# Optimization experiments

Hardware: AMD Instinct MI355X
Metric: run time of the kernel (lower is better)

## Reference

```python
import jax, jax.numpy as jnp
import numpy as np

N_HEADS = 16
N_KV_HEADS = 4
WINDOW = 128
THETA = 10000.0


def _rope_cos_sin(T, half):
    inv = 1.0 / (THETA ** (jnp.arange(half, dtype=jnp.float32) / half))
    f = jnp.arange(T, dtype=jnp.float32)[:, None] * inv[None, :]  # (T, half)
    return jnp.cos(f), jnp.sin(f)


def _apply_rope(x, cos, sin):
    # x: (B, H, T, hd); interleaved (real, imag) pairs like torch view_as_complex
    xr, xi = x[..., 0::2], x[..., 1::2]
    out_r = xr * cos - xi * sin
    out_i = xr * sin + xi * cos
    return jnp.stack([out_r, out_i], axis=-1).reshape(x.shape)


def setup_inputs() -> dict:
    key = jax.random.key(0)
    ks = jax.random.split(key, 6)
    B, T, C = 1, 4096, 2048
    kvC = (C // N_HEADS) * N_KV_HEADS
    return {
        "x": jax.random.normal(ks[0], (B, T, C), dtype=jnp.float32),
        "wq": jax.random.normal(ks[1], (C, C), dtype=jnp.float32) * 0.02,
        "wk": jax.random.normal(ks[2], (C, kvC), dtype=jnp.float32) * 0.02,
        "wv": jax.random.normal(ks[3], (C, kvC), dtype=jnp.float32) * 0.02,
        "wo": jax.random.normal(ks[4], (C, C), dtype=jnp.float32) * 0.02,
        "sink": jnp.zeros((1, N_HEADS, 1, 1), dtype=jnp.float32),
    }


def reference(x, wq, wk, wv, wo, sink):
    B, T, C = x.shape
    hd = C // N_HEADS
    n_rep = N_HEADS // N_KV_HEADS

    q = (x @ wq).reshape(B, T, N_HEADS, hd).transpose(0, 2, 1, 3)    # (B,H,T,hd)
    k = (x @ wk).reshape(B, T, N_KV_HEADS, hd).transpose(0, 2, 1, 3)  # (B,Hkv,T,hd)
    v = (x @ wv).reshape(B, T, N_KV_HEADS, hd).transpose(0, 2, 1, 3)

    cos, sin = _rope_cos_sin(T, hd // 2)  # (T, hd/2), broadcasts over (B,H,T,hd/2)
    q = _apply_rope(q, cos, sin)
    k = _apply_rope(k, cos, sin)

    # GQA head expansion (repeat_interleave over head dim)
    k = jnp.repeat(k, n_rep, axis=1)
    v = jnp.repeat(v, n_rep, axis=1)

    att = jnp.einsum("bhqd,bhkd->bhqk", q, k) * (hd ** -0.5) + sink

    # symmetric sliding-window band: |i - j| <= window//2
    idx = jnp.arange(T)
    band = jnp.abs(idx[:, None] - idx[None, :]) <= (WINDOW // 2)
    att = jnp.where(band[None, None, :, :], att, -jnp.inf)

    att = jax.nn.softmax(att, axis=-1)
    # torch code replaces NaN rows (fully-masked) with uniform; band always has diag so no-op
    att = jnp.where(jnp.isnan(att), 1.0 / T, att)

    out = jnp.einsum("bhqk,bhkd->bqhd", att, v).reshape(B, T, C)
    return out @ wo
```

## Files before the change

kernel.cpp:

```cpp
#include <hip/hip_runtime.h>
#include <stdint.h>

#define T_SEQ 4096
#define C_DIM 2048
#define HD 128

typedef unsigned short ushort_t;
typedef __attribute__((ext_vector_type(8))) short shortx8;
typedef __attribute__((ext_vector_type(4))) float floatx4;
typedef __attribute__((ext_vector_type(8))) unsigned short u16x8;
typedef __attribute__((ext_vector_type(4))) unsigned short u16x4;

__device__ __forceinline__ ushort_t f2bf(float f) {
  union { float f; uint32_t u; } v; v.f = f;
  v.u += 0x7fffu + ((v.u >> 16) & 1u);
  return (ushort_t)(v.u >> 16);
}
__device__ __forceinline__ void load_lds16(const ushort_t* g, ushort_t* l) {
  __builtin_amdgcn_global_load_lds(
      (const __attribute__((address_space(1))) unsigned int*)g,
      (__attribute__((address_space(3))) unsigned int*)l, 16, 0, 0);
}

__global__ __launch_bounds__(256) void prep_kernel(
    const float* __restrict__ wq, const float* __restrict__ wk,
    const float* __restrict__ wv, const float* __restrict__ wo,
    const float* __restrict__ x,
    ushort_t* __restrict__ BtAll, ushort_t* __restrict__ woT,
    ushort_t* __restrict__ xb) {
  const int bid = blockIdx.x;
  const int tid = threadIdx.x;
  if (bid >= 2560) {
    int i = (bid - 2560) * 256 + tid;
    float4 v = ((const float4*)x)[i];
    u16x4 o; o[0] = f2bf(v.x); o[1] = f2bf(v.y); o[2] = f2bf(v.z); o[3] = f2bf(v.w);
    ((u16x4*)xb)[i] = o;
    return;
  }
  const float* src; ushort_t* dst; int C, bx, by;
  if (bid < 1024) { src = wq; dst = BtAll; C = 2048; bx = bid & 31; by = bid >> 5; }
  else if (bid < 1280) { int b = bid - 1024; src = wk; dst = BtAll + (size_t)2048 * 2048; C = 512; bx = b & 7; by = b >> 3; }
  else if (bid < 1536) { int b = bid - 1280; src = wv; dst = BtAll + (size_t)2560 * 2048; C = 512; bx = b & 7; by = b >> 3; }
  else { int b = bid - 1536; src = wo; dst = woT; C = 2048; bx = b & 31; by = b >> 5; }
  const int R = 2048;

  __shared__ float tile[64][65];
  const int c0 = bx * 64, r0 = by * 64;
  for (int i = tid; i < 1024; i += 256) {
    int r = i >> 4, cc = (i & 15) * 4;
    float4 v = *(const float4*)&src[(size_t)(r0 + r) * C + c0 + cc];
    tile[r][cc] = v.x; tile[r][cc + 1] = v.y; tile[r][cc + 2] = v.z; tile[r][cc + 3] = v.w;
  }
  __syncthreads();
  for (int i = tid; i < 512; i += 256) {
    int oc = i >> 3;
    int g = (i & 7) * 8;
    u16x8 o;
    for (int j = 0; j < 8; ++j) o[j] = f2bf(tile[g + j][oc]);
    *(u16x8*)&dst[(size_t)(c0 + oc) * R + r0 + g] = o;
  }
}


struct GemmAcc { floatx4 a[4][4]; };

__device__ __forceinline__ void gemm_core_bk64(
    const ushort_t* __restrict__ A, const ushort_t* __restrict__ Bt,
    ushort_t* As, ushort_t* Bs, GemmAcc& acc,
    int m0, int n0, int K, int tid, int lane, int wave, int quad, int l16,
    int wm, int wn) {
  const int nk = K >> 6;
  for (int kk = 0; kk < nk; ++kk) {
    const int k0 = kk << 6;
    for (int r = 0; r < 4; ++r) {
      int e = r * 256 + tid;
      int row = e >> 3;
      int p = e & 7;
      int g = (p - row) & 7;
      const ushort_t* ga = A + (size_t)(m0 + row) * K + k0 + g * 8;
      const ushort_t* gb = Bt + (size_t)(n0 + row) * K + k0 + g * 8;
      ushort_t* la = As + (size_t)(r * 256 + (tid & 192)) * 8;
      ushort_t* lb = Bs + (size_t)(r * 256 + (tid & 192)) * 8;
      load_lds16(ga, la);
      load_lds16(gb, lb);
    }
    __syncthreads();
    for (int ks = 0; ks < 2; ++ks) {
      shortx8 af[4], bfr[4];
      for (int i = 0; i < 4; ++i) {
        int ar = wm + i * 16 + l16;
        af[i] = *(const shortx8*)(As + ar * 64 + (((ks << 2) + quad + ar) & 7) * 8);
        int br = wn + i * 16 + l16;
        bfr[i] = *(const shortx8*)(Bs + br * 64 + (((ks << 2) + quad + br) & 7) * 8);
      }
      for (int i = 0; i < 4; ++i)
        for (int j = 0; j < 4; ++j)
          acc.a[i][j] = __builtin_amdgcn_mfma_f32_16x16x32_bf16(af[i], bfr[j], acc.a[i][j], 0, 0, 0);
    }
    __syncthreads();
  }
}

__global__ __launch_bounds__(256, 3) void gemm_qkv(
    const ushort_t* __restrict__ A, const ushort_t* __restrict__ Bt,
    ushort_t* __restrict__ qbb, ushort_t* __restrict__ kbb,
    ushort_t* __restrict__ vtb) {
  __shared__ __align__(16) ushort_t As[128 * 64];
  __shared__ __align__(16) ushort_t Bs[128 * 64];
  const int tid = threadIdx.x;
  const int lane = tid & 63;
  const int wave = tid >> 6;
  const int quad = lane >> 4;
  const int l16 = lane & 15;
  const int m0 = blockIdx.y * 128;
  const int n0 = blockIdx.x * 128;
  const int wm = (wave & 1) * 64;
  const int wn = (wave >> 1) * 64;

  GemmAcc acc = {};
  gemm_core_bk64(A, Bt, As, Bs, acc, m0, n0, 2048, tid, lane, wave, quad, l16, wm, wn);

  if (blockIdx.x < 20) {
    const bool isq = (blockIdx.x < 16);
    const int par = l16 & 1;
    for (int j = 0; j < 4; ++j) {
      int col = n0 + wn + j * 16 + l16;
      int irot = (col & 127) >> 1;
      float inv = __expf(-0.14391157f * (float)irot);
      for (int i = 0; i < 4; ++i) {
        int t0r = m0 + wm + i * 16 + quad * 4;
        for (int r = 0; r < 4; ++r) {
          float val = acc.a[i][j][r];
          float other = __shfl_xor(val, 1, 64);
          float sn, cs;
          __sincosf((float)(t0r + r) * inv, &sn, &cs);
          float outv = par ? (other * sn + val * cs) : (val * cs - other * sn);
          if (isq) qbb[(size_t)(t0r + r) * 2048 + col] = f2bf(outv);
          else     kbb[(size_t)(t0r + r) * 512 + (col - 2048)] = f2bf(outv);
        }
      }
    }
  } else {
    for (int j = 0; j < 4; ++j) {
      int dim = n0 + wn + j * 16 + l16 - 2560;
      for (int i = 0; i < 4; ++i) {
        int t0r = m0 + wm + i * 16 + quad * 4;
        u16x4 o;
        for (int r = 0; r < 4; ++r) o[r] = f2bf(acc.a[i][j][r]);
        *(u16x4*)&vtb[(size_t)dim * T_SEQ + t0r] = o;
      }
    }
  }
}

__global__ __launch_bounds__(256, 3) void gemm_bf16(
    const ushort_t* __restrict__ A, const ushort_t* __restrict__ Bt,
    float* __restrict__ C, int M, int N, int K) {
  __shared__ __align__(16) ushort_t As[128 * 64];
  __shared__ __align__(16) ushort_t Bs[128 * 64];
  const int tid = threadIdx.x;
  const int lane = tid & 63;
  const int wave = tid >> 6;
  const int quad = lane >> 4;
  const int l16 = lane & 15;
  const int m0 = blockIdx.y * 128;
  const int n0 = blockIdx.x * 128;
  const int wm = (wave & 1) * 64;
  const int wn = (wave >> 1) * 64;

  GemmAcc acc = {};
  gemm_core_bk64(A, Bt, As, Bs, acc, m0, n0, K, tid, lane, wave, quad, l16, wm, wn);

  for (int i = 0; i < 4; ++i)
    for (int j = 0; j < 4; ++j) {
      int col = n0 + wn + j * 16 + l16;
      int rbase = m0 + wm + i * 16 + quad * 4;
      for (int r = 0; r < 4; ++r)
        C[(size_t)(rbase + r) * N + col] = acc.a[i][j][r];
    }
}

__global__ __launch_bounds__(256, 3) void attn_kernel(
    const ushort_t* __restrict__ qbb, const ushort_t* __restrict__ kbb,
    const ushort_t* __restrict__ vtb, ushort_t* __restrict__ ao) {
  __shared__ __align__(16) ushort_t QP[32 * 160];
  __shared__ __align__(16) ushort_t KV[160 * 136];
  __shared__ float redmax[2][32];
  __shared__ float redsum[2][32];

  const int tid = threadIdx.x;
  const int lane = tid & 63;
  const int wave = tid >> 6;
  const int l16 = lane & 15;
  const int quad = lane >> 4;
  const int h = blockIdx.x;
  const int kvh = h >> 2;
  const int t0 = blockIdx.y * 32;
  const int kstart = t0 - 64;
  const int qh = wave & 1;
  const int khalf = wave >> 1;
  const float scale = 0.08838834764831845f;

  for (int c = tid; c < 512; c += 256) {
    int row = c >> 4, c8 = c & 15;
    u16x8 v = *(const u16x8*)&qbb[(size_t)(t0 + row) * C_DIM + h * HD + c8 * 8];
    *(u16x8*)&QP[row * 136 + c8 * 8] = v;
  }
  for (int c = tid; c < 2560; c += 256) {
    int row = c >> 4, c8 = c & 15;
    int t = kstart + row;
    u16x8 v;
    if (t >= 0 && t < T_SEQ) {
      v = *(const u16x8*)&kbb[(size_t)t * 512 + kvh * HD + c8 * 8];
    } else {
      for (int z = 0; z < 8; ++z) v[z] = 0;
    }
    *(u16x8*)&KV[row * 136 + c8 * 8] = v;
  }
  __syncthreads();

  floatx4 acc[5] = {};
  const int arow = qh * 16 + l16;
  for (int ks = 0; ks < 4; ++ks) {
    shortx8 af = *(const shortx8*)&QP[arow * 136 + ks * 32 + quad * 8];
    for (int kt = 0; kt < 5; ++kt) {
      int brow = khalf * 80 + kt * 16 + l16;
      shortx8 bf = *(const shortx8*)&KV[brow * 136 + ks * 32 + quad * 8];
      acc[kt] = __builtin_amdgcn_mfma_f32_16x16x32_bf16(af, bf, acc[kt], 0, 0, 0);
    }
  }

  float mrow[4] = {-3e38f, -3e38f, -3e38f, -3e38f};
  for (int kt = 0; kt < 5; ++kt) {
    int col = khalf * 80 + kt * 16 + l16;
    int kg = kstart + col;
    for (int r = 0; r < 4; ++r) {
      int row = qh * 16 + quad * 4 + r;
      bool valid = (kg >= 0) && (kg < T_SEQ) && (col >= row) && (col <= row + 128);
      float s = valid ? acc[kt][r] * scale : -3e38f;
      acc[kt][r] = s;
      mrow[r] = fmaxf(mrow[r], s);
    }
  }
  for (int off = 1; off < 16; off <<= 1)
    for (int r = 0; r < 4; ++r)
      mrow[r] = fmaxf(mrow[r], __shfl_xor(mrow[r], off, 64));
  if (l16 == 0)
    for (int r = 0; r < 4; ++r)
      redmax[khalf][qh * 16 + quad * 4 + r] = mrow[r];
  __syncthreads();

  float sum4[4];
  for (int r = 0; r < 4; ++r) {
    int row = qh * 16 + quad * 4 + r;
    float m = fmaxf(redmax[0][row], redmax[1][row]);
    float s = 0.f;
    for (int kt = 0; kt < 5; ++kt) {
      float p = expf(acc[kt][r] - m);
      acc[kt][r] = p;
      s += p;
    }
    sum4[r] = s;
  }
  for (int off = 1; off < 16; off <<= 1)
    for (int r = 0; r < 4; ++r) sum4[r] += __shfl_xor(sum4[r], off, 64);
  if (l16 == 0)
    for (int r = 0; r < 4; ++r)
      redsum[khalf][qh * 16 + quad * 4 + r] = sum4[r];

  for (int kt = 0; kt < 5; ++kt) {
    int col = khalf * 80 + kt * 16 + l16;
    for (int r = 0; r < 4; ++r) {
      int row = qh * 16 + quad * 4 + r;
      QP[row * 160 + col] = f2bf(acc[kt][r]);
    }
  }

  for (int c = tid; c < 2560; c += 256) {
    int row = c / 20, c8 = c % 20;
    int k0 = kstart + c8 * 8;
    const ushort_t* g = &vtb[(size_t)(kvh * HD + row) * T_SEQ];
    u16x8 v;
    if (k0 >= 0 && k0 + 7 < T_SEQ) {
      v = *(const u16x8*)&g[k0];
    } else {
      for (int z = 0; z < 8; ++z) {
        int kk = k0 + z;
        v[z] = (kk >= 0 && kk < T_SEQ) ? g[kk] : (ushort_t)0;
      }
    }
    *(u16x8*)&KV[row * 160 + c8 * 8] = v;
  }
  __syncthreads();

  floatx4 oacc[4] = {};
  const int prow = qh * 16 + l16;
  for (int ks = 0; ks < 5; ++ks) {
    shortx8 pf = *(const shortx8*)&QP[prow * 160 + ks * 32 + quad * 8];
    for (int dt = 0; dt < 4; ++dt) {
      int vrow = khalf * 64 + dt * 16 + l16;
      shortx8 vf = *(const shortx8*)&KV[vrow * 160 + ks * 32 + quad * 8];
      oacc[dt] = __builtin_amdgcn_mfma_f32_16x16x32_bf16(pf, vf, oacc[dt], 0, 0, 0);
    }
  }

  for (int r = 0; r < 4; ++r) {
    int row = qh * 16 + quad * 4 + r;
    float rl = 1.0f / (redsum[0][row] + redsum[1][row]);
    for (int dt = 0; dt < 4; ++dt) {
      int dim = khalf * 64 + dt * 16 + l16;
      ao[(size_t)(t0 + row) * C_DIM + h * HD + dim] = f2bf(oacc[dt][r] * rl);
    }
  }
}

extern "C" void kernel_launch(void* const* d_in, const int* in_sizes, int n_in,
                              void* d_out, int out_size, void* d_ws, size_t ws_size,
                              hipStream_t stream) {
  const float* x  = (const float*)d_in[0];
  const float* wq = (const float*)d_in[1];
  const float* wk = (const float*)d_in[2];
  const float* wv = (const float*)d_in[3];
  const float* wo = (const float*)d_in[4];
  float* out = (float*)d_out;

  char* ws = (char*)d_ws;
  ushort_t* BtAll = (ushort_t*)(ws);
  ushort_t* woT   = (ushort_t*)(ws + 12582912);
  ushort_t* xb    = (ushort_t*)(ws + 20971520);
  ushort_t* qbb   = (ushort_t*)(ws + 37748736);
  ushort_t* kbb   = (ushort_t*)(ws + 54525952);
  ushort_t* vtb   = (ushort_t*)(ws + 58720256);
  ushort_t* ao    = (ushort_t*)(ws + 62914560);

  prep_kernel<<<10752, 256, 0, stream>>>(wq, wk, wv, wo, x, BtAll, woT, xb);

  gemm_qkv<<<dim3(24, 32), 256, 0, stream>>>(xb, BtAll, qbb, kbb, vtb);

  attn_kernel<<<dim3(16, 128), 256, 0, stream>>>(qbb, kbb, vtb, ao);

  gemm_bf16<<<dim3(16, 32), 256, 0, stream>>>(ao, woT, out, 4096, 2048, 2048);
}
```

Before: 263.3 us.

## Process two query heads per attention block sharing one K/V tile load

The attention kernel now handles two query heads that share a KV head in each block, halving the grid and halving the K and V global loads per query head. Each wave owns full key rows for one head and 16 queries, so the cross-wave max/sum reductions through LDS and one barrier are removed, and normalization is folded into P before the PV matmul. LDS rows are padded to a stride of 168 to change bank mapping. LDS use and register pressure rise, and launch bounds drop occupancy from 3 to 2 blocks per CU.

```diff
diff --git a/kernel.cpp b/kernel.cpp
--- a/kernel.cpp
+++ b/kernel.cpp
@@ -60,7 +60,6 @@
     *(u16x8*)&dst[(size_t)(c0 + oc) * R + r0 + g] = o;
   }
 }
-
 
 struct GemmAcc { floatx4 a[4][4]; };
 
@@ -180,31 +179,32 @@
     }
 }
 
-__global__ __launch_bounds__(256, 3) void attn_kernel(
+#define LSTR 168
+__global__ __launch_bounds__(256, 2) void attn_kernel(
     const ushort_t* __restrict__ qbb, const ushort_t* __restrict__ kbb,
     const ushort_t* __restrict__ vtb, ushort_t* __restrict__ ao) {
-  __shared__ __align__(16) ushort_t QP[32 * 160];
-  __shared__ __align__(16) ushort_t KV[160 * 136];
-  __shared__ float redmax[2][32];
-  __shared__ float redsum[2][32];
+  __shared__ __align__(16) ushort_t QP[64 * LSTR];
+  __shared__ __align__(16) ushort_t KV[160 * LSTR];
 
   const int tid = threadIdx.x;
   const int lane = tid & 63;
   const int wave = tid >> 6;
   const int l16 = lane & 15;
   const int quad = lane >> 4;
-  const int h = blockIdx.x;
-  const int kvh = h >> 2;
+  const int h0 = blockIdx.x * 2;
+  const int kvh = h0 >> 2;
   const int t0 = blockIdx.y * 32;
   const int kstart = t0 - 64;
-  const int qh = wave & 1;
-  const int khalf = wave >> 1;
+  const int hsel = wave & 1;
+  const int qh = wave >> 1;
   const float scale = 0.08838834764831845f;
 
-  for (int c = tid; c < 512; c += 256) {
+  for (int c = tid; c < 1024; c += 256) {
     int row = c >> 4, c8 = c & 15;
-    u16x8 v = *(const u16x8*)&qbb[(size_t)(t0 + row) * C_DIM + h * HD + c8 * 8];
-    *(u16x8*)&QP[row * 136 + c8 * 8] = v;
+    int h = h0 + (row >> 5);
+    int q = t0 + (row & 31);
+    u16x8 v = *(const u16x8*)&qbb[(size_t)q * C_DIM + h * HD + c8 * 8];
+    *(u16x8*)&QP[row * LSTR + c8 * 8] = v;
   }
   for (int c = tid; c < 2560; c += 256) {
     int row = c >> 4, c8 = c & 15;
@@ -215,24 +215,23 @@
     } else {
       for (int z = 0; z < 8; ++z) v[z] = 0;
     }
-    *(u16x8*)&KV[row * 136 + c8 * 8] = v;
+    *(u16x8*)&KV[row * LSTR + c8 * 8] = v;
   }
   __syncthreads();
 
-  floatx4 acc[5] = {};
-  const int arow = qh * 16 + l16;
+  floatx4 acc[10] = {};
+  const int arow = hsel * 32 + qh * 16 + l16;
   for (int ks = 0; ks < 4; ++ks) {
-    shortx8 af = *(const shortx8*)&QP[arow * 136 + ks * 32 + quad * 8];
-    for (int kt = 0; kt < 5; ++kt) {
-      int brow = khalf * 80 + kt * 16 + l16;
-      shortx8 bf = *(const shortx8*)&KV[brow * 136 + ks * 32 + quad * 8];
+    shortx8 af = *(const shortx8*)&QP[arow * LSTR + ks * 32 + quad * 8];
+    for (int kt = 0; kt < 10; ++kt) {
+      shortx8 bf = *(const shortx8*)&KV[(kt * 16 + l16) * LSTR + ks * 32 + quad * 8];
       acc[kt] = __builtin_amdgcn_mfma_f32_16x16x32_bf16(af, bf, acc[kt], 0, 0, 0);
     }
   }
 
   float mrow[4] = {-3e38f, -3e38f, -3e38f, -3e38f};
-  for (int kt = 0; kt < 5; ++kt) {
-    int col = khalf * 80 + kt * 16 + l16;
+  for (int kt = 0; kt < 10; ++kt) {
+    int col = kt * 16 + l16;
     int kg = kstart + col;
     for (int r = 0; r < 4; ++r) {
       int row = qh * 16 + quad * 4 + r;
@@ -245,41 +244,33 @@
   for (int off = 1; off < 16; off <<= 1)
     for (int r = 0; r < 4; ++r)
       mrow[r] = fmaxf(mrow[r], __shfl_xor(mrow[r], off, 64));
-  if (l16 == 0)
-    for (int r = 0; r < 4; ++r)
-      redmax[khalf][qh * 16 + quad * 4 + r] = mrow[r];
-  __syncthreads();
-
-  float sum4[4];
+  float rl[4];
   for (int r = 0; r < 4; ++r) {
-    int row = qh * 16 + quad * 4 + r;
-    float m = fmaxf(redmax[0][row], redmax[1][row]);
     float s = 0.f;
-    for (int kt = 0; kt < 5; ++kt) {
-      float p = expf(acc[kt][r] - m);
+    for (int kt = 0; kt < 10; ++kt) {
+      float p = expf(acc[kt][r] - mrow[r]);
       acc[kt][r] = p;
       s += p;
     }
-    sum4[r] = s;
+    rl[r] = s;
   }
   for (int off = 1; off < 16; off <<= 1)
-    for (int r = 0; r < 4; ++r) sum4[r] += __shfl_xor(sum4[r], off, 64);
-  if (l16 == 0)
-    for (int r = 0; r < 4; ++r)
-      redsum[khalf][qh * 16 + quad * 4 + r] = sum4[r];
-
-  for (int kt = 0; kt < 5; ++kt) {
-    int col = khalf * 80 + kt * 16 + l16;
+    for (int r = 0; r < 4; ++r) rl[r] += __shfl_xor(rl[r], off, 64);
+  for (int r = 0; r < 4; ++r) rl[r] = 1.0f / rl[r];
+
+  __syncthreads();
+
+  for (int kt = 0; kt < 10; ++kt) {
+    int col = kt * 16 + l16;
     for (int r = 0; r < 4; ++r) {
-      int row = qh * 16 + quad * 4 + r;
-      QP[row * 160 + col] = f2bf(acc[kt][r]);
-    }
-  }
-
+      int row = hsel * 32 + qh * 16 + quad * 4 + r;
+      QP[row * LSTR + col] = f2bf(acc[kt][r] * rl[r]);
+    }
+  }
   for (int c = tid; c < 2560; c += 256) {
-    int row = c / 20, c8 = c % 20;
+    int dim = c / 20, c8 = c % 20;
     int k0 = kstart + c8 * 8;
-    const ushort_t* g = &vtb[(size_t)(kvh * HD + row) * T_SEQ];
+    const ushort_t* g = &vtb[(size_t)(kvh * HD + dim) * T_SEQ];
     u16x8 v;
     if (k0 >= 0 && k0 + 7 < T_SEQ) {
       v = *(const u16x8*)&g[k0];
@@ -289,27 +280,26 @@
         v[z] = (kk >= 0 && kk < T_SEQ) ? g[kk] : (ushort_t)0;
       }
     }
-    *(u16x8*)&KV[row * 160 + c8 * 8] = v;
+    *(u16x8*)&KV[dim * LSTR + c8 * 8] = v;
   }
   __syncthreads();
 
-  floatx4 oacc[4] = {};
-  const int prow = qh * 16 + l16;
+  floatx4 oacc[8] = {};
+  const int prow = hsel * 32 + qh * 16 + l16;
   for (int ks = 0; ks < 5; ++ks) {
-    shortx8 pf = *(const shortx8*)&QP[prow * 160 + ks * 32 + quad * 8];
-    for (int dt = 0; dt < 4; ++dt) {
-      int vrow = khalf * 64 + dt * 16 + l16;
-      shortx8 vf = *(const shortx8*)&KV[vrow * 160 + ks * 32 + quad * 8];
+    shortx8 pf = *(const shortx8*)&QP[prow * LSTR + ks * 32 + quad * 8];
+    for (int dt = 0; dt < 8; ++dt) {
+      shortx8 vf = *(const shortx8*)&KV[(dt * 16 + l16) * LSTR + ks * 32 + quad * 8];
       oacc[dt] = __builtin_amdgcn_mfma_f32_16x16x32_bf16(pf, vf, oacc[dt], 0, 0, 0);
     }
   }
 
+  const int h = h0 + hsel;
   for (int r = 0; r < 4; ++r) {
-    int row = qh * 16 + quad * 4 + r;
-    float rl = 1.0f / (redsum[0][row] + redsum[1][row]);
-    for (int dt = 0; dt < 4; ++dt) {
-      int dim = khalf * 64 + dt * 16 + l16;
-      ao[(size_t)(t0 + row) * C_DIM + h * HD + dim] = f2bf(oacc[dt][r] * rl);
+    int row = t0 + qh * 16 + quad * 4 + r;
+    for (int dt = 0; dt < 8; ++dt) {
+      int dim = dt * 16 + l16;
+      ao[(size_t)row * C_DIM + h * HD + dim] = f2bf(oacc[dt][r]);
     }
   }
 }
@@ -337,7 +327,7 @@
 
   gemm_qkv<<<dim3(24, 32), 256, 0, stream>>>(xb, BtAll, qbb, kbb, vtb);
 
-  attn_kernel<<<dim3(16, 128), 256, 0, stream>>>(qbb, kbb, vtb, ao);
+  attn_kernel<<<dim3(8, 128), 256, 0, stream>>>(qbb, kbb, vtb, ao);
 
   gemm_bf16<<<dim3(16, 32), 256, 0, stream>>>(ao, woT, out, 4096, 2048, 2048);
 }
```

Result: faster. 243.0 us (-7.7%).
